# Kernel tuning notes

Measured on AMD Instinct MI355X. Metric: run time of the kernel, lower is better.

The kernel has to match this reference:

```python
import jax, jax.numpy as jnp
import numpy as np

B, C, H, W = 8, 256, 96, 96
HEADS, WS = 8, 12
HD = C // HEADS
SCALE = HD ** -0.5
L = WS * WS  # tokens per window


def _rel_index(ws):
    # Swin-style relative position index, computed statically (matches torch.meshgrid 'ij')
    coords = np.stack(np.meshgrid(np.arange(ws), np.arange(ws), indexing='ij')).reshape(2, -1)
    rel = (coords[:, :, None] - coords[:, None, :]).transpose(1, 2, 0) + (ws - 1)
    return rel[..., 0] * (2 * ws - 1) + rel[..., 1]  # [L, L]

REL_IDX = jnp.asarray(_rel_index(WS).reshape(-1))


def dct1(x):
    # 1D DCT-II along last axis via rfft, matches the torch implementation
    n = x.shape[-1]
    xv = jnp.concatenate([x, x[..., ::-1]], axis=-1)
    X = jnp.fft.rfft(xv, axis=-1)[..., :n]
    k = jnp.arange(n, dtype=jnp.float32)
    Wc = jnp.exp(-1j * jnp.pi * k / (2 * n))
    return (X * Wc).real.astype(jnp.float32)


def dct2(x):
    x = dct1(x.swapaxes(-1, -2)).swapaxes(-1, -2)
    return dct1(x)


def idct1(X):
    n = X.shape[-1]
    k = jnp.arange(n, dtype=jnp.float32)
    Wc = jnp.exp(1j * jnp.pi * k / (2 * n))
    Xc = X.astype(jnp.complex64) * Wc
    Xc_full = jnp.concatenate([Xc, Xc[..., 1:-1][..., ::-1]], axis=-1)
    # irfft with n=2n crops input to n+1 bins, exactly like torch.fft.irfft
    x = jnp.fft.irfft(Xc_full, n=2 * n, axis=-1)
    return x[..., :n].astype(jnp.float32)


def idct2(x):
    x = idct1(x.swapaxes(-1, -2)).swapaxes(-1, -2)
    return idct1(x)


def conv2d(x, w, groups=1, pad=0):
    return jax.lax.conv_general_dilated(
        x, w, (1, 1), [(pad, pad), (pad, pad)],
        dimension_numbers=('NCHW', 'OIHW', 'NCHW'), feature_group_count=groups)


def batchnorm(x, g, b):
    # training-mode BN (module default): per-batch statistics over (B,H,W)
    m = x.mean(axis=(0, 2, 3), keepdims=True)
    v = x.var(axis=(0, 2, 3), keepdims=True)
    return (x - m) * jax.lax.rsqrt(v + 1e-5) * g.reshape(1, -1, 1, 1) + b.reshape(1, -1, 1, 1)


def setup_inputs() -> dict:
    key = jax.random.key(0)
    ks = jax.random.split(key, 10)
    def rn(k, shape, s=0.02):
        return jax.random.normal(k, shape, dtype=jnp.float32) * s
    return {
        'x': jax.random.normal(ks[0], (B, C, H, W), dtype=jnp.float32),
        'qkv_w': rn(ks[1], (3 * C, C)), 'qkv_b': jnp.zeros((3 * C,), jnp.float32),
        'proj_w': rn(ks[2], (C, C)), 'proj_b': jnp.zeros((C,), jnp.float32),
        'lpe_w': rn(ks[3], (C, 1, 3, 3), 0.1), 'lpe_b': jnp.zeros((C,), jnp.float32),
        'lpe_scale': jnp.ones((1,), jnp.float32),
        'rpb_table': rn(ks[4], ((2 * WS - 1) ** 2, HEADS), 0.02),
        'ec_w': rn(ks[5], (1, 1, 3, 3), 0.3),
        'bn1_g': jnp.ones((1,), jnp.float32), 'bn1_b': jnp.zeros((1,), jnp.float32),
        'nl_w': rn(ks[6], (1, 1), 1.0), 'nl_b': jnp.zeros((1,), jnp.float32),
        'fr_w': rn(ks[7], (C, C, 1, 1), 0.05),
        'bn2_g': jnp.ones((C,), jnp.float32), 'bn2_b': jnp.zeros((C,), jnp.float32),
    }


def reference(x, qkv_w, qkv_b, proj_w, proj_b, lpe_w, lpe_b, lpe_scale, rpb_table,
              ec_w, bn1_g, bn1_b, nl_w, nl_b, fr_w, bn2_g, bn2_b):
    # ---- FreqNoiseDetector ----
    freq = jnp.abs(dct2(x))                                      # [B,C,H,W]
    mn = freq.min(axis=(2, 3), keepdims=True)
    mx = freq.max(axis=(2, 3), keepdims=True)
    freq_norm = (freq - mn) / (mx + 1e-6)
    local_energy = jax.nn.relu(batchnorm(
        conv2d(freq_norm.mean(axis=1, keepdims=True), ec_w, pad=1), bn1_g, bn1_b))  # [B,1,H,W]
    pooled = local_energy.mean(axis=(2, 3))                      # [B,1]
    noise_global = jax.nn.sigmoid(pooled @ nl_w.T + nl_b)        # [B,1]
    noise_mask = jax.nn.sigmoid(1.0 - local_energy) * noise_global.reshape(B, 1, 1, 1)

    # ---- DynamicAttention: SW-MSA with relative position bias ----
    xh = x.transpose(0, 2, 3, 1)                                 # [B,H,W,C]
    win = xh.reshape(B, H // WS, WS, W // WS, WS, C).transpose(0, 1, 3, 2, 4, 5).reshape(-1, L, C)
    qkv = (win @ qkv_w.T + qkv_b).reshape(-1, L, 3, HEADS, HD).transpose(2, 0, 3, 1, 4)
    q, k, v = qkv[0], qkv[1], qkv[2]                             # [Bw,h,L,hd]
    attn = jnp.einsum('bhld,bhmd->bhlm', q, k) * SCALE
    bias = rpb_table[REL_IDX].reshape(L, L, HEADS).transpose(2, 0, 1)
    attn = jax.nn.softmax(attn + bias[None], axis=-1)
    out = jnp.einsum('bhlm,bhmd->bhld', attn, v).transpose(0, 2, 1, 3).reshape(-1, L, C)
    out = out @ proj_w.T + proj_b
    x_attn = out.reshape(B, H // WS, W // WS, WS, WS, C).transpose(0, 1, 3, 2, 4, 5).reshape(B, H, W, C)
    # noise-guided depthwise LPE
    x_lpe = (conv2d(x, lpe_w, groups=C, pad=1) + lpe_b.reshape(1, C, 1, 1)) * lpe_scale * noise_mask
    x_attn_img = x_attn.transpose(0, 3, 1, 2) + x_lpe            # [B,C,H,W]

    # ---- frequency soft gate ----
    freq2 = dct2(x_attn_img)
    freq_mean = freq2.mean(axis=(2, 3), keepdims=True)
    gate = jax.nn.sigmoid(5.0 * (jnp.abs(freq2) - freq_mean))
    x_freq = idct2(freq2 * gate)

    # ---- 1x1 refine + residual ----
    y = batchnorm(conv2d(x + x_freq, fr_w), bn2_g, bn2_b)
    return jax.nn.gelu(y, approximate=False)
```

## Files before the change

### kernel.cpp

```cpp
#include <hip/hip_runtime.h>
#include <math.h>

#define Bb     8
#define Cc     256
#define Hh     96
#define Ww     96
#define HEADS  8
#define WS_    12
#define HD     32
#define LL     144
#define NPIX   9216
#define NPLANE 2048
#define NTOK   73728
#define NWIN   512
#define SCALE_ 0.17677669529663687f
#define BN1N   73728.0f
#define GELC   0.7071067811865476f

#define OFF_DT    0
#define OFF_MT    9216
#define OFF_FNM   18432
#define OFF_E     92160
#define OFF_MASK  165888
#define OFF_P3    239616
#define OFF_ST1   240192
#define OFF_BN2   240200
#define OFF_BUF0  262144
#define OFF_BUF1  19136512
#define OFF_BUF2  38010880

#define QKV_TSEC 4718592

static __device__ __forceinline__ float sigm(float x){ return 1.0f/(1.0f+__expf(-x)); }

__global__ void k_mat(float* Dt, float* Mt){
  int t = blockIdx.x*256 + threadIdx.x;
  if (t < 9216){
    int k = t/96, i = t%96;
    Dt[t] = (float)(2.0*cos(3.14159265358979323846*(double)i*(double)(2*k+1)/192.0));
  } else if (t < 18432){
    int u = t - 9216;
    int k = u/96, j = u%96;
    double v = (k==0) ? 1.0 : 2.0*cos(3.14159265358979323846*(double)k*(double)(2*j+1)/192.0);
    if (k == 94) v += cos(3.14159265358979323846*94.0/192.0) * ((j&1)? -1.0 : 1.0);
    Mt[u] = (float)(v/192.0);
  }
}

__global__ __launch_bounds__(256) void k_plane(const float* __restrict__ in, float* __restrict__ out,
                                               const float* __restrict__ Pt, const float* __restrict__ Qt,
                                               int mode){
  __shared__ __align__(16) float Ts[96*98];
  __shared__ __align__(16) float SA[1536];
  __shared__ __align__(16) float SB[1536];
  const int plane = blockIdx.x;
  const int tid = threadIdx.x;
  const int ti = tid>>4, tx = tid&15;
  const int i0 = ti*6, j0 = tx*6;
  const float* src = in + (size_t)plane*NPIX;

  float acc[6][6];
  #pragma unroll
  for (int a=0;a<6;++a){
    #pragma unroll
    for (int b=0;b<6;++b) acc[a][b]=0.f;
  }

  for (int kc=0; kc<6; ++kc){
    for (int t=tid; t<1536; t+=256){ SA[t] = src[kc*1536+t]; SB[t] = Pt[kc*1536+t]; }
    __syncthreads();
    #pragma unroll
    for (int k=0;k<16;++k){
      float2 a0 = *(const float2*)&SB[k*96+i0];
      float2 a1 = *(const float2*)&SB[k*96+i0+2];
      float2 a2 = *(const float2*)&SB[k*96+i0+4];
      float2 b0 = *(const float2*)&SA[k*96+j0];
      float2 b1 = *(const float2*)&SA[k*96+j0+2];
      float2 b2 = *(const float2*)&SA[k*96+j0+4];
      float av[6] = {a0.x,a0.y,a1.x,a1.y,a2.x,a2.y};
      float bv[6] = {b0.x,b0.y,b1.x,b1.y,b2.x,b2.y};
      #pragma unroll
      for (int ii=0;ii<6;++ii){
        #pragma unroll
        for (int jj=0;jj<6;++jj) acc[ii][jj] = fmaf(av[ii], bv[jj], acc[ii][jj]);
      }
    }
    __syncthreads();
  }
  #pragma unroll
  for (int jj=0;jj<6;++jj){
    #pragma unroll
    for (int ii=0;ii<6;++ii) Ts[(j0+jj)*98 + i0+ii] = acc[ii][jj];
  }
  __syncthreads();

  float y[6][6];
  #pragma unroll
  for (int a=0;a<6;++a){
    #pragma unroll
    for (int b=0;b<6;++b) y[a][b]=0.f;
  }

  for (int kc=0; kc<6; ++kc){
    for (int t=tid; t<1536; t+=256) SA[t] = Qt[kc*1536+t];
    __syncthreads();
    #pragma unroll
    for (int k=0;k<16;++k){
      int kg = kc*16+k;
      float2 a0 = *(const float2*)&Ts[kg*98+i0];
      float2 a1 = *(const float2*)&Ts[kg*98+i0+2];
      float2 a2 = *(const float2*)&Ts[kg*98+i0+4];
      float2 b0 = *(const float2*)&SA[k*96+j0];
      float2 b1 = *(const float2*)&SA[k*96+j0+2];
      float2 b2 = *(const float2*)&SA[k*96+j0+4];
      float av[6] = {a0.x,a0.y,a1.x,a1.y,a2.x,a2.y};
      float bv[6] = {b0.x,b0.y,b1.x,b1.y,b2.x,b2.y};
      #pragma unroll
      for (int ii=0;ii<6;++ii){
        #pragma unroll
        for (int jj=0;jj<6;++jj) y[ii][jj] = fmaf(av[ii], bv[jj], y[ii][jj]);
      }
    }
    __syncthreads();
  }

  float* dst = out + (size_t)plane*NPIX;
  if (mode == 0){
    float lmn = 3.4e38f, lmx = 0.f;
    #pragma unroll
    for (int ii=0;ii<6;++ii){
      #pragma unroll
      for (int jj=0;jj<6;++jj){ float a=fabsf(y[ii][jj]); lmn=fminf(lmn,a); lmx=fmaxf(lmx,a); }
    }
    SB[tid]=lmn; SB[256+tid]=lmx; __syncthreads();
    for (int o=128;o;o>>=1){
      if (tid<o){ SB[tid]=fminf(SB[tid],SB[tid+o]); SB[256+tid]=fmaxf(SB[256+tid],SB[256+tid+o]); }
      __syncthreads();
    }
    float mn = SB[0], inv = 1.f/(SB[256]+1e-6f);
    #pragma unroll
    for (int ii=0;ii<6;++ii){
      #pragma unroll
      for (int jj=0;jj<6;++jj) dst[(i0+ii)*96 + j0+jj] = (fabsf(y[ii][jj])-mn)*inv;
    }
  } else if (mode == 1){
    float ls = 0.f;
    #pragma unroll
    for (int ii=0;ii<6;++ii){
      #pragma unroll
      for (int jj=0;jj<6;++jj) ls += y[ii][jj];
    }
    SB[tid]=ls; __syncthreads();
    for (int o=128;o;o>>=1){ if (tid<o) SB[tid]+=SB[tid+o]; __syncthreads(); }
    float mean = SB[0]*(1.f/9216.f);
    #pragma unroll
    for (int ii=0;ii<6;++ii){
      #pragma unroll
      for (int jj=0;jj<6;++jj){
        float v = y[ii][jj];
        dst[(i0+ii)*96 + j0+jj] = v * sigm(5.f*(fabsf(v)-mean));
      }
    }
  } else {
    #pragma unroll
    for (int ii=0;ii<6;++ii){
      #pragma unroll
      for (int jj=0;jj<6;++jj) dst[(i0+ii)*96 + j0+jj] = y[ii][jj];
    }
  }
}

__global__ void k_chmean(const float* __restrict__ A, float* __restrict__ FNM){
  int px = blockIdx.x*256 + threadIdx.x;
  int b = px/NPIX, p = px - b*NPIX;
  const float* base = A + (size_t)b*Cc*NPIX + p;
  float s = 0.f;
  #pragma unroll 8
  for (int c=0;c<Cc;++c) s += base[(size_t)c*NPIX];
  FNM[px] = s*(1.f/256.f);
}

__global__ void k_conv3(const float* __restrict__ FNM, const float* __restrict__ w9,
                        float* __restrict__ E, float* __restrict__ P3){
  __shared__ float rs[256], rq[256];
  int px = blockIdx.x*256 + threadIdx.x;
  int b = px/NPIX, p = px - b*NPIX;
  int h = p/96, w = p - h*96;
  const float* base = FNM + b*NPIX;
  float a = 0.f;
  #pragma unroll
  for (int dy=0;dy<3;++dy){
    int hh = h+dy-1;
    if (hh>=0 && hh<96){
      #pragma unroll
      for (int dx=0;dx<3;++dx){
        int ww2 = w+dx-1;
        if (ww2>=0 && ww2<96) a = fmaf(base[hh*96+ww2], w9[dy*3+dx], a);
      }
    }
  }
  E[px] = a;
  rs[threadIdx.x]=a; rq[threadIdx.x]=a*a; __syncthreads();
  for (int o=128;o;o>>=1){
    if (threadIdx.x<o){ rs[threadIdx.x]+=rs[threadIdx.x+o]; rq[threadIdx.x]+=rq[threadIdx.x+o]; }
    __syncthreads();
  }
  if (threadIdx.x==0){ P3[2*blockIdx.x]=rs[0]; P3[2*blockIdx.x+1]=rq[0]; }
}

__global__ void k_red576(const float* __restrict__ P3, float* __restrict__ ST1){
  __shared__ float rs[256], rq[256];
  float s=0.f,q=0.f;
  for (int i=threadIdx.x;i<288;i+=256){ s+=P3[2*i]; q+=P3[2*i+1]; }
  rs[threadIdx.x]=s; rq[threadIdx.x]=q; __syncthreads();
  for (int o=128;o;o>>=1){
    if (threadIdx.x<o){ rs[threadIdx.x]+=rs[threadIdx.x+o]; rq[threadIdx.x]+=rq[threadIdx.x+o]; }
    __syncthreads();
  }
  if (threadIdx.x==0){ ST1[0]=rs[0]; ST1[1]=rq[0]; }
}

__global__ void k_mask(const float* __restrict__ E, const float* __restrict__ ST1,
                       const float* __restrict__ g1, const float* __restrict__ b1,
                       const float* __restrict__ nw, const float* __restrict__ nb,
                       float* __restrict__ MASK){
  __shared__ float les[NPIX];
  __shared__ float red[256];
  int b = blockIdx.x, tid = threadIdx.x;
  float m = ST1[0]*(1.f/BN1N);
  float v = ST1[1]*(1.f/BN1N) - m*m;
  float rstd = rsqrtf(v + 1e-5f);
  float ga = g1[0], be = b1[0];
  float local = 0.f;
  for (int p=tid;p<NPIX;p+=256){
    float le = fmaxf(0.f, (E[b*NPIX+p]-m)*rstd*ga + be);
    les[p] = le; local += le;
  }
  red[tid]=local; __syncthreads();
  for (int o=128;o;o>>=1){ if (tid<o) red[tid]+=red[tid+o]; __syncthreads(); }
  float ng = sigm(red[0]*(1.f/9216.f)*nw[0] + nb[0]);
  for (int p=tid;p<NPIX;p+=256)
    MASK[b*NPIX+p] = sigm(1.f - les[p]) * ng;
}

__global__ void k_tr(const float* __restrict__ x, float* __restrict__ XT){
  __shared__ float tile[32][33];
  int pt = blockIdx.x*32, ct = blockIdx.y*32, b = blockIdx.z;
  int txd = threadIdx.x, tyd = threadIdx.y;
  #pragma unroll
  for (int q=0;q<4;++q){
    int c = ct + tyd + q*8;
    tile[tyd+q*8][txd] = x[(size_t)(b*Cc+c)*NPIX + pt + txd];
  }
  __syncthreads();
  #pragma unroll
  for (int q=0;q<4;++q){
    int p = pt + tyd + q*8;
    XT[(size_t)(b*NPIX+p)*Cc + ct + txd] = tile[txd][tyd+q*8];
  }
}

__global__ __launch_bounds__(256) void k_qkv(const float* __restrict__ XT, const float* __restrict__ Wq,
                                             const float* __restrict__ bq, float* __restrict__ qkv, int g){
  __shared__ __align__(16) float As[16*128];
  __shared__ __align__(16) float Bs[16*96];
  const int mt = blockIdx.x, nt = blockIdx.y;
  const int r0 = mt*128;
  const int tid = threadIdx.x;
  const int ty = tid>>4, tx = tid&15;
  float acc[8][6];
  #pragma unroll
  for (int a=0;a<8;++a){
    #pragma unroll
    for (int b=0;b<6;++b) acc[a][b]=0.f;
  }

  for (int k0=0;k0<256;k0+=16){
    #pragma unroll
    for (int it=0;it<2;++it){
      int f = tid + it*256;
      int i = f>>2, kq = f&3;
      int r = r0 + i;
      int win = r/144, l = r - win*144;
      int b = win>>6, wh = (win>>3)&7, wwi = win&7;
      int lh = l/12, lw = l - lh*12;
      int pix = (wh*12+lh)*96 + wwi*12+lw;
      float4 v = *(const float4*)&XT[((size_t)((b*NPIX)+pix))*256 + k0 + (kq<<2)];
      int kk = kq<<2;
      As[(kk+0)*128+i]=v.x; As[(kk+1)*128+i]=v.y; As[(kk+2)*128+i]=v.z; As[(kk+3)*128+i]=v.w;
    }
    #pragma unroll
    for (int it=0;it<2;++it){
      int f = tid + it*256;
      if (f < 384){
        int c = f>>2, kq = f&3;
        int cg = nt*96 + c;
        int t = cg>>6, hl = (cg>>5)&1, d = cg&31;
        int wrow = t*256 + (g*2+hl)*32 + d;
        float4 v = *(const float4*)&Wq[(size_t)wrow*256 + k0 + (kq<<2)];
        int kk = kq<<2;
        Bs[(kk+0)*96+c]=v.x; Bs[(kk+1)*96+c]=v.y; Bs[(kk+2)*96+c]=v.z; Bs[(kk+3)*96+c]=v.w;
      }
    }
    __syncthreads();
    #pragma unroll
    for (int k=0;k<16;++k){
      const float4* pa = (const float4*)&As[k*128 + ty*8];
      float4 a0 = pa[0], a1 = pa[1];
      float av[8] = {a0.x,a0.y,a0.z,a0.w,a1.x,a1.y,a1.z,a1.w};
      const float2* pb = (const float2*)&Bs[k*96];
      float2 b0 = pb[tx], b1 = pb[tx+16], b2 = pb[tx+32];
      float bv[6] = {b0.x,b0.y,b1.x,b1.y,b2.x,b2.y};
      #pragma unroll
      for (int ii=0;ii<8;++ii){
        #pragma unroll
        for (int jj=0;jj<6;++jj) acc[ii][jj] = fmaf(av[ii], bv[jj], acc[ii][jj]);
      }
    }
    __syncthreads();
  }
  #pragma unroll
  for (int ii=0;ii<8;++ii){
    int r = r0 + ty*8 + ii;
    int win = r/144, l = r - win*144;
    #pragma unroll
    for (int jj=0;jj<6;++jj){
      int s = jj>>1;
      int c = nt*96 + 2*tx + s*32 + (jj&1);
      int t = c>>6, hl = (c>>5)&1, d = c&31;
      float val = acc[ii][jj] + bq[t*256 + (g*2+hl)*32 + d];
      qkv[(size_t)t*QKV_TSEC + ((size_t)(win*2+hl)*144 + l)*32 + d] = val;
    }
  }
}

__global__ __launch_bounds__(192) void k_attn(const float* __restrict__ qkv, const float* __restrict__ rpb,
                                              float* __restrict__ O, int g){
  __shared__ __align__(16) float qt[32*144];
  __shared__ __align__(16) float Ks[144*32];
  __shared__ __align__(16) float Vs[144*32];
  __shared__ float rpbs[532];
  const int win = blockIdx.x, hl = blockIdx.y;
  const int head = g*2 + hl;
  const int tid = threadIdx.x;
  const float* Qg = qkv + ((size_t)(win*2+hl)*144)*32;
  const float* Kg = Qg + QKV_TSEC;
  const float* Vg = Qg + 2*(size_t)QKV_TSEC;
  for (int t=tid; t<4608; t+=192){
    Ks[t] = Kg[t]; Vs[t] = Vg[t];
    int l = t>>5, d = t&31;
    qt[d*144+l] = Qg[t];
  }
  for (int t=tid; t<529; t+=192) rpbs[t] = rpb[t*8 + head];
  __syncthreads();

  int r = tid;
  if (r < 144){
    float q[32];
    #pragma unroll
    for (int d=0;d<32;++d) q[d] = qt[d*144+r];
    float o[32];
    #pragma unroll
    for (int d=0;d<32;++d) o[d]=0.f;
    float m = -3.4e38f, sum = 0.f;
    int rh = r/12, rw = r - rh*12;
    int jh = 0, jw = 0;
    for (int j=0;j<144;++j){
      const float4* kp = (const float4*)&Ks[j*32];
      float s0=0,s1=0,s2=0,s3=0;
      #pragma unroll
      for (int t=0;t<8;++t){
        float4 kv = kp[t];
        s0 = fmaf(q[4*t+0],kv.x,s0); s1 = fmaf(q[4*t+1],kv.y,s1);
        s2 = fmaf(q[4*t+2],kv.z,s2); s3 = fmaf(q[4*t+3],kv.w,s3);
      }
      float s = ((s0+s1)+(s2+s3))*SCALE_ + rpbs[(rh-jh+11)*23 + (rw-jw+11)];
      float mn2 = fmaxf(m, s);
      if (mn2 > m){
        float corr = __expf(m - mn2);
        sum *= corr;
        #pragma unroll
        for (int d=0;d<32;++d) o[d]*=corr;
        m = mn2;
      }
      float p = __expf(s - m);
      sum += p;
      const float4* vp = (const float4*)&Vs[j*32];
      #pragma unroll
      for (int t=0;t<8;++t){
        float4 vv = vp[t];
        o[4*t+0]=fmaf(p,vv.x,o[4*t+0]); o[4*t+1]=fmaf(p,vv.y,o[4*t+1]);
        o[4*t+2]=fmaf(p,vv.z,o[4*t+2]); o[4*t+3]=fmaf(p,vv.w,o[4*t+3]);
      }
      if (++jw==12){ jw=0; ++jh; }
    }
    float inv = 1.f/sum;
    float* dst = O + ((size_t)(win*144+r))*256 + head*32;
    #pragma unroll
    for (int t=0;t<8;++t){
      float4 t4 = { o[4*t]*inv, o[4*t+1]*inv, o[4*t+2]*inv, o[4*t+3]*inv };
      *(float4*)&dst[4*t] = t4;
    }
  }
}

__global__ void k_lpe(const float* __restrict__ x, const float* __restrict__ lw,
                      const float* __restrict__ lb, const float* __restrict__ ls,
                      const float* __restrict__ MASK, float* __restrict__ Y1){
  float scale = ls[0];
  for (size_t idx = (size_t)blockIdx.x*256 + threadIdx.x; idx < (size_t)Bb*Cc*NPIX; idx += (size_t)gridDim.x*256){
    int pc = (int)(idx/NPIX); int p = (int)(idx - (size_t)pc*NPIX);
    int b = pc>>8, c = pc&255;
    int h = p/96, w = p - h*96;
    const float* xp = x + (size_t)pc*NPIX;
    const float* wp = lw + c*9;
    float a = 0.f;
    #pragma unroll
    for (int dy=0;dy<3;++dy){
      int hh = h+dy-1;
      if (hh>=0 && hh<96){
        #pragma unroll
        for (int dx=0;dx<3;++dx){
          int ww2 = w+dx-1;
          if (ww2>=0 && ww2<96) a = fmaf(xp[hh*96+ww2], wp[dy*3+dx], a);
        }
      }
    }
    Y1[idx] += (a + lb[c]) * scale * MASK[b*NPIX+p];
  }
}

__global__ __launch_bounds__(256) void k_proj(const float* __restrict__ O, const float* __restrict__ Wp,
                                              const float* __restrict__ bp, float* __restrict__ PROJ){
  __shared__ __align__(16) float As[16*128];
  __shared__ __align__(16) float Bs[16*128];
  const int mt = blockIdx.x, nt = blockIdx.y;
  const int r0 = mt*128, c0 = nt*128;
  const int tid = threadIdx.x;
  const int ty = tid>>4, tx = tid&15;
  float acc[8][8];
  #pragma unroll
  for (int a=0;a<8;++a){
    #pragma unroll
    for (int b=0;b<8;++b) acc[a][b]=0.f;
  }

  for (int k0=0;k0<256;k0+=16){
    #pragma unroll
    for (int it=0;it<2;++it){
      int f = tid + it*256;
      int i = f>>2, kq = f&3;
      float4 v = *(const float4*)&O[((size_t)(r0+i))*256 + k0 + (kq<<2)];
      int kk = kq<<2;
      As[(kk+0)*128+i]=v.x; As[(kk+1)*128+i]=v.y; As[(kk+2)*128+i]=v.z; As[(kk+3)*128+i]=v.w;
    }
    #pragma unroll
    for (int it=0;it<2;++it){
      int f = tid + it*256;
      int c = f>>2, kq = f&3;
      float4 v = *(const float4*)&Wp[((size_t)(c0+c))*256 + k0 + (kq<<2)];
      int kk = kq<<2;
      Bs[(kk+0)*128+c]=v.x; Bs[(kk+1)*128+c]=v.y; Bs[(kk+2)*128+c]=v.z; Bs[(kk+3)*128+c]=v.w;
    }
    __syncthreads();
    #pragma unroll
    for (int k=0;k<16;++k){
      const float4* pa = (const float4*)&As[k*128 + ty*8];
      float4 a0 = pa[0], a1 = pa[1];
      float av[8] = {a0.x,a0.y,a0.z,a0.w,a1.x,a1.y,a1.z,a1.w};
      const float4* pb = (const float4*)&Bs[k*128];
      float4 b0 = pb[tx], b1 = pb[tx+16];
      float bv[8] = {b0.x,b0.y,b0.z,b0.w,b1.x,b1.y,b1.z,b1.w};
      #pragma unroll
      for (int ii=0;ii<8;++ii){
        #pragma unroll
        for (int jj=0;jj<8;++jj) acc[ii][jj] = fmaf(av[ii], bv[jj], acc[ii][jj]);
      }
    }
    __syncthreads();
  }
  const float4 bp0 = *(const float4*)&bp[c0 + 4*tx];
  const float4 bp1 = *(const float4*)&bp[c0 + 64 + 4*tx];
  #pragma unroll
  for (int ii=0;ii<8;++ii){
    int r = r0 + ty*8 + ii;
    float* pp = PROJ + (size_t)r*256 + c0;
    float4 v0 = { acc[ii][0]+bp0.x, acc[ii][1]+bp0.y, acc[ii][2]+bp0.z, acc[ii][3]+bp0.w };
    float4 v1 = { acc[ii][4]+bp1.x, acc[ii][5]+bp1.y, acc[ii][6]+bp1.z, acc[ii][7]+bp1.w };
    *(float4*)&pp[4*tx] = v0;
    *(float4*)&pp[64 + 4*tx] = v1;
  }
}

__global__ __launch_bounds__(256) void k_merge(const float* __restrict__ PROJ, float* __restrict__ Y1){
  __shared__ float T[96*65];
  const int bx = blockIdx.x;
  const int b = bx/96, h = bx - b*96;
  const int wh = h/12, lh = h - wh*12;
  const int c0 = blockIdx.y*64;
  const int t = threadIdx.x;
  const int wave = t>>6, lane = t&63;
  for (int it=0; it<24; ++it){
    int tok = wave*24 + it;
    int wwi = tok/12, lw = tok - wwi*12;
    int gtok = (b*64 + wh*8 + wwi)*144 + lh*12 + lw;
    T[tok*65 + lane] = PROJ[(size_t)gtok*256 + c0 + lane];
  }
  __syncthreads();
  const int cl = t>>2, p0 = (t&3)*24;
  float* dst = Y1 + ((size_t)(b*Cc + c0 + cl))*NPIX + h*96 + p0;
  #pragma unroll
  for (int i=0;i<24;i+=4){
    float4 v = { T[(p0+i)*65+cl], T[(p0+i+1)*65+cl], T[(p0+i+2)*65+cl], T[(p0+i+3)*65+cl] };
    *(float4*)&dst[i] = v;
  }
}

__global__ __launch_bounds__(256) void k_conv1x1(const float* __restrict__ x, const float* __restrict__ XF,
                                                 const float* __restrict__ Wf, float* __restrict__ Z){
  __shared__ __align__(16) float As[16*128];
  __shared__ __align__(16) float Bs[16*128];
  const int mt = blockIdx.x, nt = blockIdx.y;
  const int gp0 = mt*128;
  const int b = gp0/NPIX, p0 = gp0 - b*NPIX;
  const int c0 = nt*128;
  const int tid = threadIdx.x;
  const int ty = tid>>4, tx = tid&15;
  float acc[8][8];
  #pragma unroll
  for (int a=0;a<8;++a){
    #pragma unroll
    for (int bb=0;bb<8;++bb) acc[a][bb]=0.f;
  }

  for (int k0=0;k0<256;k0+=16){
    #pragma unroll
    for (int it=0;it<2;++it){
      int f = tid + it*256;
      int k = f>>5, i4 = f&31;
      size_t off = ((size_t)(b*Cc + k0 + k))*NPIX + p0 + i4*4;
      float4 va = *(const float4*)&x[off];
      float4 vb = *(const float4*)&XF[off];
      float4 s = { va.x+vb.x, va.y+vb.y, va.z+vb.z, va.w+vb.w };
      *(float4*)&As[k*128 + i4*4] = s;
    }
    #pragma unroll
    for (int it=0;it<2;++it){
      int f = tid + it*256;
      int c = f>>2, kq = f&3;
      float4 v = *(const float4*)&Wf[((size_t)(c0+c))*256 + k0 + (kq<<2)];
      int kk = kq<<2;
      Bs[(kk+0)*128+c]=v.x; Bs[(kk+1)*128+c]=v.y; Bs[(kk+2)*128+c]=v.z; Bs[(kk+3)*128+c]=v.w;
    }
    __syncthreads();
    #pragma unroll
    for (int k=0;k<16;++k){
      const float4* pa = (const float4*)&As[k*128 + ty*8];
      float4 a0 = pa[0], a1 = pa[1];
      float av[8] = {a0.x,a0.y,a0.z,a0.w,a1.x,a1.y,a1.z,a1.w};
      const float4* pb = (const float4*)&Bs[k*128];
      float4 b0 = pb[tx], b1 = pb[tx+16];
      float bv[8] = {b0.x,b0.y,b0.z,b0.w,b1.x,b1.y,b1.z,b1.w};
      #pragma unroll
      for (int ii=0;ii<8;++ii){
        #pragma unroll
        for (int jj=0;jj<8;++jj) acc[ii][jj] = fmaf(av[ii], bv[jj], acc[ii][jj]);
      }
    }
    __syncthreads();
  }
  #pragma unroll
  for (int jj=0;jj<8;++jj){
    int co = c0 + ((jj<4)? 4*tx+jj : 64 + 4*tx + (jj-4));
    float4 lo = {acc[0][jj],acc[1][jj],acc[2][jj],acc[3][jj]};
    float4 hi = {acc[4][jj],acc[5][jj],acc[6][jj],acc[7][jj]};
    float* zp = Z + ((size_t)(b*Cc+co))*NPIX + p0 + ty*8;
    *(float4*)zp = lo;
    *(float4*)(zp+4) = hi;
  }
}

__global__ void k_bnstat(const float* __restrict__ Z, float* __restrict__ BN2){
  __shared__ float rs[256], rq[256];
  int c = blockIdx.x, tid = threadIdx.x;
  float s=0.f,q=0.f;
  for (int b=0;b<Bb;++b){
    const float* pl = Z + ((size_t)(b*Cc+c))*NPIX;
    for (int i=tid;i<NPIX/4;i+=256){
      float4 v = *(const float4*)&pl[i*4];
      s += v.x+v.y+v.z+v.w;
      q += v.x*v.x + v.y*v.y + v.z*v.z + v.w*v.w;
    }
  }
  rs[tid]=s; rq[tid]=q; __syncthreads();
  for (int o=128;o;o>>=1){
    if (tid<o){ rs[tid]+=rs[tid+o]; rq[tid]+=rq[tid+o]; }
    __syncthreads();
  }
  if (tid==0){ BN2[c]=rs[0]; BN2[256+c]=rq[0]; }
}

__global__ void k_final(const float* __restrict__ Z, const float* __restrict__ BN2,
                        const float* __restrict__ g2, const float* __restrict__ b2,
                        float* __restrict__ out){
  size_t f4 = (size_t)blockIdx.x*256 + threadIdx.x;
  size_t base = f4*4;
  int c = (int)((base/NPIX) & 255);
  float m = BN2[c]*(1.f/BN1N);
  float v = BN2[256+c]*(1.f/BN1N) - m*m;
  float rstd = rsqrtf(v+1e-5f);
  float ga = g2[c], be = b2[c];
  float4 z = *(const float4*)&Z[base];
  float4 r;
  float y;
  y = (z.x-m)*rstd*ga + be; r.x = 0.5f*y*(1.f+erff(y*GELC));
  y = (z.y-m)*rstd*ga + be; r.y = 0.5f*y*(1.f+erff(y*GELC));
  y = (z.z-m)*rstd*ga + be; r.z = 0.5f*y*(1.f+erff(y*GELC));
  y = (z.w-m)*rstd*ga + be; r.w = 0.5f*y*(1.f+erff(y*GELC));
  *(float4*)&out[base] = r;
}

extern "C" void kernel_launch(void* const* d_in, const int* in_sizes, int n_in,
                              void* d_out, int out_size, void* d_ws, size_t ws_size,
                              hipStream_t stream){
  const float* x      = (const float*)d_in[0];
  const float* qkv_w  = (const float*)d_in[1];
  const float* qkv_b  = (const float*)d_in[2];
  const float* proj_w = (const float*)d_in[3];
  const float* proj_b = (const float*)d_in[4];
  const float* lpe_w  = (const float*)d_in[5];
  const float* lpe_b  = (const float*)d_in[6];
  const float* lpe_s  = (const float*)d_in[7];
  const float* rpb    = (const float*)d_in[8];
  const float* ec_w   = (const float*)d_in[9];
  const float* bn1_g  = (const float*)d_in[10];
  const float* bn1_b  = (const float*)d_in[11];
  const float* nl_w   = (const float*)d_in[12];
  const float* nl_b   = (const float*)d_in[13];
  const float* fr_w   = (const float*)d_in[14];
  const float* bn2_g  = (const float*)d_in[15];
  const float* bn2_b  = (const float*)d_in[16];
  float* outp = (float*)d_out;

  float* WS   = (float*)d_ws;
  float* Dt   = WS + OFF_DT;
  float* Mt   = WS + OFF_MT;
  float* FNM  = WS + OFF_FNM;
  float* E    = WS + OFF_E;
  float* MASK = WS + OFF_MASK;
  float* P3   = WS + OFF_P3;
  float* ST1  = WS + OFF_ST1;
  float* BN2  = WS + OFF_BN2;
  float* BUF0 = WS + OFF_BUF0;
  float* BUF1 = WS + OFF_BUF1;
  float* BUF2 = WS + OFF_BUF2;

  k_mat<<<72,256,0,stream>>>(Dt, Mt);
  k_plane<<<NPLANE,256,0,stream>>>(x, BUF2, Dt, Dt, 0);
  k_chmean<<<288,256,0,stream>>>(BUF2, FNM);
  k_conv3<<<288,256,0,stream>>>(FNM, ec_w, E, P3);
  k_red576<<<1,256,0,stream>>>(P3, ST1);
  k_mask<<<8,256,0,stream>>>(E, ST1, bn1_g, bn1_b, nl_w, nl_b, MASK);
  k_tr<<<dim3(288,8,8),dim3(32,8),0,stream>>>(x, BUF0);
  for (int g=0; g<4; ++g){
    k_qkv<<<dim3(576,2),256,0,stream>>>(BUF0, qkv_w, qkv_b, BUF1, g);
    k_attn<<<dim3(512,2),192,0,stream>>>(BUF1, rpb, BUF2, g);
  }
  k_proj<<<dim3(576,2),256,0,stream>>>(BUF2, proj_w, proj_b, BUF0);
  k_merge<<<dim3(768,4),256,0,stream>>>(BUF0, BUF1);
  k_lpe<<<4096,256,0,stream>>>(x, lpe_w, lpe_b, lpe_s, MASK, BUF1);
  k_plane<<<NPLANE,256,0,stream>>>(BUF1, BUF2, Dt, Dt, 1);
  k_plane<<<NPLANE,256,0,stream>>>(BUF2, BUF0, Mt, Mt, 2);
  k_conv1x1<<<dim3(576,2),256,0,stream>>>(x, BUF0, fr_w, BUF1);
  k_bnstat<<<256,256,0,stream>>>(BUF1, BN2);
  k_final<<<18432,256,0,stream>>>(BUF1, BN2, bn2_g, bn2_b, outp);
}
```

Baseline: 2.137 ms.

## Run 2D DCT plane transforms on MFMA with split-bf16 emulated fp32

The per-plane 96x96 DCT/IDCT matrix products move from scalar FP32 FMA register tiles onto bf16 MFMA instructions. Each FP32 operand is split into high and low bf16 parts and multiplied with three MFMAs to keep close to FP32 accuracy. The basis matrices are precomputed in a fragment-ready swizzled layout, and the intermediate transpose stays in shared memory as split bf16. The aim is to cut the ALU cost of the three k_plane launches, at the price of slightly lower precision (the lo*lo term is dropped) and more complex data layouts.

```diff
diff --git a/kernel.cpp b/kernel.cpp
--- a/kernel.cpp
+++ b/kernel.cpp
@@ -18,7 +18,6 @@
 #define GELC   0.7071067811865476f
 
 #define OFF_DT    0
-#define OFF_MT    9216
 #define OFF_FNM   18432
 #define OFF_E     92160
 #define OFF_MASK  165888
@@ -31,141 +30,185 @@
 
 #define QKV_TSEC 4718592
 
+typedef short bf16x8 __attribute__((ext_vector_type(8)));
+typedef short s16x4  __attribute__((ext_vector_type(4)));
+typedef float f32x4  __attribute__((ext_vector_type(4)));
+
 static __device__ __forceinline__ float sigm(float x){ return 1.0f/(1.0f+__expf(-x)); }
 
-__global__ void k_mat(float* Dt, float* Mt){
+static __device__ __forceinline__ void split2(float f, short& h, short& l){
+  unsigned u = __float_as_uint(f);
+  unsigned hb = u & 0xffff0000u;
+  h = (short)(hb>>16);
+  float lo = f - __uint_as_float(hb);
+  l = (short)(__float_as_uint(lo)>>16);
+}
+
+__global__ void k_mat(short* DFh, short* DFl, short* MFh, short* MFl){
   int t = blockIdx.x*256 + threadIdx.x;
-  if (t < 9216){
-    int k = t/96, i = t%96;
-    Dt[t] = (float)(2.0*cos(3.14159265358979323846*(double)i*(double)(2*k+1)/192.0));
-  } else if (t < 18432){
-    int u = t - 9216;
-    int k = u/96, j = u%96;
-    double v = (k==0) ? 1.0 : 2.0*cos(3.14159265358979323846*(double)k*(double)(2*j+1)/192.0);
-    if (k == 94) v += cos(3.14159265358979323846*94.0/192.0) * ((j&1)? -1.0 : 1.0);
-    Mt[u] = (float)(v/192.0);
-  }
+  int m = t/9216, u = t - m*9216;
+  int k = u/96, n = u - k*96;
+  double v;
+  if (m == 0){
+    v = 2.0*cos(3.14159265358979323846*(double)n*(double)(2*k+1)/192.0);
+  } else {
+    v = (k==0) ? 1.0 : 2.0*cos(3.14159265358979323846*(double)k*(double)(2*n+1)/192.0);
+    if (k == 94) v += cos(3.14159265358979323846*94.0/192.0) * ((n&1)? -1.0 : 1.0);
+    v /= 192.0;
+  }
+  float f = (float)v;
+  short hs, ls; split2(f, hs, ls);
+  int kt = k>>5, lr = (k>>3)&3, jj = k&7, nt = n>>4;
+  int idx = ((kt*6+nt)*64 + (lr*16 + (n&15)))*8 + jj;
+  if (m == 0){ DFh[idx]=hs; DFl[idx]=ls; }
+  else       { MFh[idx]=hs; MFl[idx]=ls; }
 }
 
 __global__ __launch_bounds__(256) void k_plane(const float* __restrict__ in, float* __restrict__ out,
-                                               const float* __restrict__ Pt, const float* __restrict__ Qt,
+                                               const short* __restrict__ Fh, const short* __restrict__ Fl,
                                                int mode){
-  __shared__ __align__(16) float Ts[96*98];
-  __shared__ __align__(16) float SA[1536];
-  __shared__ __align__(16) float SB[1536];
-  const int plane = blockIdx.x;
+  __shared__ __align__(16) short Xh[96*104];
+  __shared__ __align__(16) short Xl[96*104];
+  __shared__ float red[512];
   const int tid = threadIdx.x;
-  const int ti = tid>>4, tx = tid&15;
-  const int i0 = ti*6, j0 = tx*6;
-  const float* src = in + (size_t)plane*NPIX;
-
-  float acc[6][6];
-  #pragma unroll
-  for (int a=0;a<6;++a){
-    #pragma unroll
-    for (int b=0;b<6;++b) acc[a][b]=0.f;
-  }
-
-  for (int kc=0; kc<6; ++kc){
-    for (int t=tid; t<1536; t+=256){ SA[t] = src[kc*1536+t]; SB[t] = Pt[kc*1536+t]; }
-    __syncthreads();
-    #pragma unroll
-    for (int k=0;k<16;++k){
-      float2 a0 = *(const float2*)&SB[k*96+i0];
-      float2 a1 = *(const float2*)&SB[k*96+i0+2];
-      float2 a2 = *(const float2*)&SB[k*96+i0+4];
-      float2 b0 = *(const float2*)&SA[k*96+j0];
-      float2 b1 = *(const float2*)&SA[k*96+j0+2];
-      float2 b2 = *(const float2*)&SA[k*96+j0+4];
-      float av[6] = {a0.x,a0.y,a1.x,a1.y,a2.x,a2.y};
-      float bv[6] = {b0.x,b0.y,b1.x,b1.y,b2.x,b2.y};
-      #pragma unroll
-      for (int ii=0;ii<6;++ii){
-        #pragma unroll
-        for (int jj=0;jj<6;++jj) acc[ii][jj] = fmaf(av[ii], bv[jj], acc[ii][jj]);
-      }
-    }
-    __syncthreads();
-  }
-  #pragma unroll
-  for (int jj=0;jj<6;++jj){
-    #pragma unroll
-    for (int ii=0;ii<6;++ii) Ts[(j0+jj)*98 + i0+ii] = acc[ii][jj];
+  const int lane = tid & 63, wid = tid >> 6;
+  const int l15 = lane & 15, l4 = lane >> 4;
+  const float* src = in + (size_t)blockIdx.x*NPIX;
+
+  for (int t4 = tid; t4 < 576; t4 += 256){
+    int rt = t4/24, ct = t4 - rt*24;
+    const float* p0 = src + rt*4*96 + ct*4;
+    float4 v0 = *(const float4*)(p0);
+    float4 v1 = *(const float4*)(p0+96);
+    float4 v2 = *(const float4*)(p0+192);
+    float4 v3 = *(const float4*)(p0+288);
+#define STCOL(f0,f1,f2,f3,j) { s16x4 hv, lv; short hs, ls; \
+    split2(f0,hs,ls); hv[0]=hs; lv[0]=ls; \
+    split2(f1,hs,ls); hv[1]=hs; lv[1]=ls; \
+    split2(f2,hs,ls); hv[2]=hs; lv[2]=ls; \
+    split2(f3,hs,ls); hv[3]=hs; lv[3]=ls; \
+    int cc = ct*4+(j); \
+    *(s16x4*)&Xh[cc*104 + rt*4] = hv; \
+    *(s16x4*)&Xl[cc*104 + rt*4] = lv; }
+    STCOL(v0.x,v1.x,v2.x,v3.x,0)
+    STCOL(v0.y,v1.y,v2.y,v3.y,1)
+    STCOL(v0.z,v1.z,v2.z,v3.z,2)
+    STCOL(v0.w,v1.w,v2.w,v3.w,3)
+#undef STCOL
   }
   __syncthreads();
 
-  float y[6][6];
-  #pragma unroll
-  for (int a=0;a<6;++a){
-    #pragma unroll
-    for (int b=0;b<6;++b) y[a][b]=0.f;
-  }
-
-  for (int kc=0; kc<6; ++kc){
-    for (int t=tid; t<1536; t+=256) SA[t] = Qt[kc*1536+t];
-    __syncthreads();
-    #pragma unroll
-    for (int k=0;k<16;++k){
-      int kg = kc*16+k;
-      float2 a0 = *(const float2*)&Ts[kg*98+i0];
-      float2 a1 = *(const float2*)&Ts[kg*98+i0+2];
-      float2 a2 = *(const float2*)&Ts[kg*98+i0+4];
-      float2 b0 = *(const float2*)&SA[k*96+j0];
-      float2 b1 = *(const float2*)&SA[k*96+j0+2];
-      float2 b2 = *(const float2*)&SA[k*96+j0+4];
-      float av[6] = {a0.x,a0.y,a1.x,a1.y,a2.x,a2.y};
-      float bv[6] = {b0.x,b0.y,b1.x,b1.y,b2.x,b2.y};
-      #pragma unroll
-      for (int ii=0;ii<6;++ii){
-        #pragma unroll
-        for (int jj=0;jj<6;++jj) y[ii][jj] = fmaf(av[ii], bv[jj], y[ii][jj]);
-      }
-    }
-    __syncthreads();
-  }
-
-  float* dst = out + (size_t)plane*NPIX;
-  if (mode == 0){
+  f32x4 acc[9];
+  #pragma unroll
+  for (int t=0;t<9;++t) acc[t] = (f32x4){0.f,0.f,0.f,0.f};
+
+  #pragma unroll
+  for (int t=0;t<9;++t){
+    int gt = wid*9 + t;
+    int mt = gt/6, nt = gt - mt*6;
+    int arow = mt*16 + l15;
+    #pragma unroll
+    for (int kb=0;kb<3;++kb){
+      bf16x8 ah = *(const bf16x8*)&Xh[arow*104 + kb*32 + l4*8];
+      bf16x8 al = *(const bf16x8*)&Xl[arow*104 + kb*32 + l4*8];
+      const bf16x8 bh = *(const bf16x8*)(Fh + (size_t)((kb*6+nt)*64 + lane)*8);
+      const bf16x8 bl = *(const bf16x8*)(Fl + (size_t)((kb*6+nt)*64 + lane)*8);
+      acc[t] = __builtin_amdgcn_mfma_f32_16x16x32_bf16(al, bh, acc[t], 0,0,0);
+      acc[t] = __builtin_amdgcn_mfma_f32_16x16x32_bf16(ah, bl, acc[t], 0,0,0);
+      acc[t] = __builtin_amdgcn_mfma_f32_16x16x32_bf16(ah, bh, acc[t], 0,0,0);
+    }
+  }
+  __syncthreads();
+
+  #pragma unroll
+  for (int t=0;t<9;++t){
+    int gt = wid*9 + t;
+    int mt = gt/6, nt = gt - mt*6;
+    int ti = nt*16 + l15, tj = mt*16 + l4*4;
+    s16x4 hv, lv; short hs, ls;
+    split2(acc[t][0],hs,ls); hv[0]=hs; lv[0]=ls;
+    split2(acc[t][1],hs,ls); hv[1]=hs; lv[1]=ls;
+    split2(acc[t][2],hs,ls); hv[2]=hs; lv[2]=ls;
+    split2(acc[t][3],hs,ls); hv[3]=hs; lv[3]=ls;
+    *(s16x4*)&Xh[ti*104+tj] = hv;
+    *(s16x4*)&Xl[ti*104+tj] = lv;
+  }
+  #pragma unroll
+  for (int t=0;t<9;++t) acc[t] = (f32x4){0.f,0.f,0.f,0.f};
+  __syncthreads();
+
+  #pragma unroll
+  for (int t=0;t<9;++t){
+    int gt = wid*9 + t;
+    int it = gt/6, jt = gt - it*6;
+    int arow = it*16 + l15;
+    #pragma unroll
+    for (int kb=0;kb<3;++kb){
+      bf16x8 ah = *(const bf16x8*)&Xh[arow*104 + kb*32 + l4*8];
+      bf16x8 al = *(const bf16x8*)&Xl[arow*104 + kb*32 + l4*8];
+      const bf16x8 bh = *(const bf16x8*)(Fh + (size_t)((kb*6+jt)*64 + lane)*8);
+      const bf16x8 bl = *(const bf16x8*)(Fl + (size_t)((kb*6+jt)*64 + lane)*8);
+      acc[t] = __builtin_amdgcn_mfma_f32_16x16x32_bf16(al, bh, acc[t], 0,0,0);
+      acc[t] = __builtin_amdgcn_mfma_f32_16x16x32_bf16(ah, bl, acc[t], 0,0,0);
+      acc[t] = __builtin_amdgcn_mfma_f32_16x16x32_bf16(ah, bh, acc[t], 0,0,0);
+    }
+  }
+
+  float* dst = out + (size_t)blockIdx.x*NPIX;
+  if (mode == 2){
+    #pragma unroll
+    for (int t=0;t<9;++t){
+      int gt = wid*9 + t;
+      int it = gt/6, jt = gt - it*6;
+      int i0 = it*16 + l4*4, j = jt*16 + l15;
+      dst[(i0+0)*96 + j] = acc[t][0];
+      dst[(i0+1)*96 + j] = acc[t][1];
+      dst[(i0+2)*96 + j] = acc[t][2];
+      dst[(i0+3)*96 + j] = acc[t][3];
+    }
+  } else if (mode == 0){
     float lmn = 3.4e38f, lmx = 0.f;
     #pragma unroll
-    for (int ii=0;ii<6;++ii){
-      #pragma unroll
-      for (int jj=0;jj<6;++jj){ float a=fabsf(y[ii][jj]); lmn=fminf(lmn,a); lmx=fmaxf(lmx,a); }
-    }
-    SB[tid]=lmn; SB[256+tid]=lmx; __syncthreads();
+    for (int t=0;t<9;++t){
+      #pragma unroll
+      for (int p=0;p<4;++p){ float a = fabsf(acc[t][p]); lmn = fminf(lmn,a); lmx = fmaxf(lmx,a); }
+    }
+    red[tid]=lmn; red[256+tid]=lmx; __syncthreads();
     for (int o=128;o;o>>=1){
-      if (tid<o){ SB[tid]=fminf(SB[tid],SB[tid+o]); SB[256+tid]=fmaxf(SB[256+tid],SB[256+tid+o]); }
+      if (tid<o){ red[tid]=fminf(red[tid],red[tid+o]); red[256+tid]=fmaxf(red[256+tid],red[256+tid+o]); }
       __syncthreads();
     }
-    float mn = SB[0], inv = 1.f/(SB[256]+1e-6f);
-    #pragma unroll
-    for (int ii=0;ii<6;++ii){
-      #pragma unroll
-      for (int jj=0;jj<6;++jj) dst[(i0+ii)*96 + j0+jj] = (fabsf(y[ii][jj])-mn)*inv;
-    }
-  } else if (mode == 1){
+    float mn = red[0], inv = 1.f/(red[256]+1e-6f);
+    #pragma unroll
+    for (int t=0;t<9;++t){
+      int gt = wid*9 + t;
+      int it = gt/6, jt = gt - it*6;
+      int i0 = it*16 + l4*4, j = jt*16 + l15;
+      dst[(i0+0)*96 + j] = (fabsf(acc[t][0])-mn)*inv;
+      dst[(i0+1)*96 + j] = (fabsf(acc[t][1])-mn)*inv;
+      dst[(i0+2)*96 + j] = (fabsf(acc[t][2])-mn)*inv;
+      dst[(i0+3)*96 + j] = (fabsf(acc[t][3])-mn)*inv;
+    }
+  } else {
     float ls = 0.f;
     #pragma unroll
-    for (int ii=0;ii<6;++ii){
-      #pragma unroll
-      for (int jj=0;jj<6;++jj) ls += y[ii][jj];
-    }
-    SB[tid]=ls; __syncthreads();
-    for (int o=128;o;o>>=1){ if (tid<o) SB[tid]+=SB[tid+o]; __syncthreads(); }
-    float mean = SB[0]*(1.f/9216.f);
-    #pragma unroll
-    for (int ii=0;ii<6;++ii){
-      #pragma unroll
-      for (int jj=0;jj<6;++jj){
-        float v = y[ii][jj];
-        dst[(i0+ii)*96 + j0+jj] = v * sigm(5.f*(fabsf(v)-mean));
-      }
-    }
-  } else {
-    #pragma unroll
-    for (int ii=0;ii<6;++ii){
-      #pragma unroll
-      for (int jj=0;jj<6;++jj) dst[(i0+ii)*96 + j0+jj] = y[ii][jj];
+    for (int t=0;t<9;++t){
+      #pragma unroll
+      for (int p=0;p<4;++p) ls += acc[t][p];
+    }
+    red[tid]=ls; __syncthreads();
+    for (int o=128;o;o>>=1){ if (tid<o) red[tid]+=red[tid+o]; __syncthreads(); }
+    float mean = red[0]*(1.f/9216.f);
+    #pragma unroll
+    for (int t=0;t<9;++t){
+      int gt = wid*9 + t;
+      int it = gt/6, jt = gt - it*6;
+      int i0 = it*16 + l4*4, j = jt*16 + l15;
+      #pragma unroll
+      for (int p=0;p<4;++p){
+        float v = acc[t][p];
+        dst[(i0+p)*96 + j] = v * sigm(5.f*(fabsf(v)-mean));
+      }
     }
   }
 }
@@ -643,8 +686,11 @@
   float* outp = (float*)d_out;
 
   float* WS   = (float*)d_ws;
-  float* Dt   = WS + OFF_DT;
-  float* Mt   = WS + OFF_MT;
+  short* FR   = (short*)(WS + OFF_DT);
+  short* DFh  = FR;
+  short* DFl  = FR + 9216;
+  short* MFh  = FR + 18432;
+  short* MFl  = FR + 27648;
   float* FNM  = WS + OFF_FNM;
   float* E    = WS + OFF_E;
   float* MASK = WS + OFF_MASK;
@@ -655,8 +701,8 @@
   float* BUF1 = WS + OFF_BUF1;
   float* BUF2 = WS + OFF_BUF2;
 
-  k_mat<<<72,256,0,stream>>>(Dt, Mt);
-  k_plane<<<NPLANE,256,0,stream>>>(x, BUF2, Dt, Dt, 0);
+  k_mat<<<72,256,0,stream>>>(DFh, DFl, MFh, MFl);
+  k_plane<<<NPLANE,256,0,stream>>>(x, BUF2, DFh, DFl, 0);
   k_chmean<<<288,256,0,stream>>>(BUF2, FNM);
   k_conv3<<<288,256,0,stream>>>(FNM, ec_w, E, P3);
   k_red576<<<1,256,0,stream>>>(P3, ST1);
@@ -669,8 +715,8 @@
   k_proj<<<dim3(576,2),256,0,stream>>>(BUF2, proj_w, proj_b, BUF0);
   k_merge<<<dim3(768,4),256,0,stream>>>(BUF0, BUF1);
   k_lpe<<<4096,256,0,stream>>>(x, lpe_w, lpe_b, lpe_s, MASK, BUF1);
-  k_plane<<<NPLANE,256,0,stream>>>(BUF1, BUF2, Dt, Dt, 1);
-  k_plane<<<NPLANE,256,0,stream>>>(BUF2, BUF0, Mt, Mt, 2);
+  k_plane<<<NPLANE,256,0,stream>>>(BUF1, BUF2, DFh, DFl, 1);
+  k_plane<<<NPLANE,256,0,stream>>>(BUF2, BUF0, MFh, MFl, 2);
   k_conv1x1<<<dim3(576,2),256,0,stream>>>(x, BUF0, fr_w, BUF1);
   k_bnstat<<<256,256,0,stream>>>(BUF1, BN2);
   k_final<<<18432,256,0,stream>>>(BUF1, BN2, bn2_g, bn2_b, outp);
```

Measured after the change: 1.828 ms. -14.5%, faster.
